# Optimization experiments

Hardware: AMD Instinct MI355X
Metric: run time of the kernel (lower is better)

## Reference

```python
import jax, jax.numpy as jnp
import numpy as np

N, H, DDE, NH = 256, 256, 64, 4

def setup_inputs() -> dict:
    key = jax.random.key(0)
    ks = jax.random.split(key, 12)
    rn = lambda k, s, sc=1.0: (jax.random.normal(k, s) * sc).astype(jnp.float32)
    return {
        "action_hidden_state": rn(ks[0], (N, H)),
        "goal_hidden_state": rn(ks[1], (N, H)),
        "goal": rn(ks[2], (N, 2)),
        "action": rn(ks[3], (N, 2)),
        "W_dist": rn(ks[4], (8, DDE), 0.3),          # distEmbedding Linear(8, dde)
        "b_dist": jnp.zeros((DDE,), jnp.float32),
        "W_gate": rn(ks[5], (DDE, H), 0.1),          # gateFC Linear(dde, H)
        "b_gate": jnp.zeros((H,), jnp.float32),
        "w": rn(ks[6], (NH, 1, H, H), 0.06),         # GAT per-head projection
        "a": rn(ks[7], (1, 1, 2 * H, 1), 0.06),      # attention vector
        "bias": jnp.zeros((H,), jnp.float32),
    }

def reference(action_hidden_state, goal_hidden_state, goal, action,
              W_dist, b_dist, W_gate, b_gate, w, a, bias):
    n = goal.shape[0]
    # --- InteractionGate.cal_gate: x1[i,j] = x[j], x2[i,j] = x[i] ---
    g1 = jnp.broadcast_to(goal[None, :, :], (n, n, 2))
    g2 = jnp.broadcast_to(goal[:, None, :], (n, n, 2))
    a1 = jnp.broadcast_to(action[None, :, :], (n, n, 2))
    a2 = jnp.broadcast_to(action[:, None, :], (n, n, 2))
    dist = jnp.concatenate([a2, g2, a1, g1], axis=-1)                 # [n,n,8]
    gate = jax.nn.sigmoid(jax.nn.relu(dist @ W_dist + b_dist) @ W_gate + b_gate)  # [n,n,H]
    # temp_action_1[i,j] = action_hidden_state[j]
    gate_action = gate * jnp.tanh(action_hidden_state[None, :, :])    # [n,n,H]
    # diagonal entries replaced by goal_hidden_state (mask_goal = eye)
    eye = jnp.eye(n, dtype=bool)[:, :, None]
    gated_h = jnp.where(eye, goal_hidden_state[None, :, :], gate_action)  # [n,n,H]

    # --- GAT assembly: h_self[i,k] = ahs[i]; h_other = cat(ahs, gated_h) ---
    h_other = jnp.concatenate([action_hidden_state[:, None, :], gated_h], axis=1)  # [n,n+1,H]

    wm = w[:, 0]          # [NH,H,H]
    a_flat = a[0, 0, :, 0]  # [2H]
    f = wm.shape[-1]
    n_head = wm.shape[0]
    # h_self rows along k are all identical -> project once per (head, node)
    hsp = jnp.einsum('nh,zhf->znf', action_hidden_state, wm)          # [NH,n,f]
    hop = jnp.einsum('nkh,zhf->znkf', h_other, wm)                    # [NH,n,n+1,f]
    # cat([h_self', h_other']) @ a  ==  h_self'@a[:f] + h_other'@a[f:]
    score = (hsp @ a_flat[:f])[:, :, None] + hop @ a_flat[f:]         # [NH,n,n+1]
    e = jnp.where(score > 0, score, 0.2 * score)                      # LeakyReLU(0.2)
    alpha = jax.nn.softmax(e, axis=-1)                                # softmax over neighbors
    # h_attn = matmul(h_other, w) == hop; weighted sum over k, mean over heads
    out = jnp.einsum('znk,znkf->nf', alpha, hop) / n_head             # [n,f]
    return jax.nn.relu(out) + bias
```

## Files before the change

kernel.cpp:

```cpp
#include <hip/hip_runtime.h>
#include <hip/hip_bf16.h>

#define NN 256
#define HH 256

typedef __attribute__((ext_vector_type(8))) short short8;
typedef __attribute__((ext_vector_type(4))) float f32x4;
typedef __attribute__((ext_vector_type(4))) unsigned short su4;

__device__ __forceinline__ ushort f2bf(float x) {
    __hip_bfloat16 h = __float2bfloat16(x);
    return *reinterpret_cast<ushort*>(&h);
}
__device__ __forceinline__ float bf2f(ushort u) {
    __hip_bfloat16 h = *reinterpret_cast<__hip_bfloat16*>(&u);
    return __bfloat162float(h);
}
template <int CTRL>
__device__ __forceinline__ float dpp_add(float x) {
    int y = __builtin_amdgcn_update_dpp(0, __float_as_int(x), CTRL, 0xF, 0xF, true);
    return x + __int_as_float(y);
}
template <int CTRL>
__device__ __forceinline__ float dpp_max(float x) {
    int y = __builtin_amdgcn_update_dpp(0, __float_as_int(x), CTRL, 0xF, 0xF, true);
    return fmaxf(x, __int_as_float(y));
}
__device__ __forceinline__ float red16(float v) {
    v = dpp_add<0xB1>(v); v = dpp_add<0x4E>(v);
    v = dpp_add<0x141>(v); v = dpp_add<0x140>(v);
    return v;
}
__device__ __forceinline__ float red16max(float v) {
    v = dpp_max<0xB1>(v); v = dpp_max<0x4E>(v);
    v = dpp_max<0x141>(v); v = dpp_max<0x140>(v);
    return v;
}

#define WS_P   0
#define WS_Q   16384
#define WS_T   32768
#define WS_WA  98304
#define WS_WB  99328
#define WS_WGT 100352
#define WS_PV  109568
#define WS_ML  1158144
#define WS_W2H 1166336
#define WS_W2L 1297408

__global__ __launch_bounds__(256) void precompute_kernel(
    const float* __restrict__ ahs, const float* __restrict__ goal,
    const float* __restrict__ action, const float* __restrict__ Wd,
    const float* __restrict__ b_dist, const float* __restrict__ Wg,
    const float* __restrict__ w, const float* __restrict__ a,
    float* __restrict__ ws)
{
    const int b = blockIdx.x;
    const int t = threadIdx.x;
    float* P  = ws + WS_P;
    float* Q  = ws + WS_Q;
    float* T  = ws + WS_T;
    float* WA = ws + WS_WA;
    float* WB = ws + WS_WB;
    ushort* WgT  = (ushort*)(ws + WS_WGT);
    ushort* W2hi = (ushort*)(ws + WS_W2H);
    ushort* W2lo = (ushort*)(ws + WS_W2L);

    __shared__ __align__(16) float tile[64][65];

    if (b < 64) {
        const int idx = (b*256 + t)*4;
        float4 v = *(const float4*)(ahs + idx);
        float4 o;
        o.x = tanhf(v.x); o.y = tanhf(v.y); o.z = tanhf(v.z); o.w = tanhf(v.w);
        *(float4*)(T + idx) = o;
    } else if (b < 128) {
        const int i = (b - 64)*4 + (t >> 6);
        const int d = t & 63;
        float a0 = action[2*i], a1 = action[2*i+1];
        float g0 = goal[2*i],   g1 = goal[2*i+1];
        P[i*64 + d] = a0*Wd[0*64+d] + a1*Wd[1*64+d]
                    + g0*Wd[2*64+d] + g1*Wd[3*64+d] + b_dist[d];
        Q[i*64 + d] = a0*Wd[4*64+d] + a1*Wd[5*64+d]
                    + g0*Wd[6*64+d] + g1*Wd[7*64+d];
    } else if (b < 144) {
        const int r    = b - 128;
        const int z    = r >> 2;
        const int rg   = r & 3;
        const int wid  = t >> 6;
        const int lane = t & 63;
        const int hbase = rg*64 + wid*16;
        const f32x4 aB = *(const f32x4*)(a + lane*4);
        const f32x4 aA = *(const f32x4*)(a + HH + lane*4);
#pragma unroll 4
        for (int rr = 0; rr < 16; ++rr) {
            const int h = hbase + rr;
            const f32x4 w4 = *(const f32x4*)(w + z*HH*HH + h*HH + lane*4);
            float dA = w4.x*aA.x + w4.y*aA.y + w4.z*aA.z + w4.w*aA.w;
            float dB = w4.x*aB.x + w4.y*aB.y + w4.z*aB.z + w4.w*aB.w;
#pragma unroll
            for (int off = 32; off; off >>= 1) {
                dA += __shfl_xor(dA, off);
                dB += __shfl_xor(dB, off);
            }
            if (lane == 0) { WA[z*HH + h] = dA; WB[z*HH + h] = dB; }
        }
    } else if (b < 208) {
        const int d = b - 144;
        WgT[t*72 + d] = f2bf(Wg[d*HH + t]);
    } else {
        const int idx = b - 208;
        const int k0  = (idx >> 2) * 64;
        const int f0  = (idx & 3) * 64;
        const int r   = t >> 6;
        const int ff  = t & 63;
#pragma unroll 4
        for (int i = 0; i < 16; ++i) {
            const int kk = i*4 + r;
            tile[kk][ff] = w[(k0 + kk)*HH + f0 + ff];
        }
        __syncthreads();
#pragma unroll 4
        for (int i = 0; i < 16; ++i) {
            const int fl = i*4 + r;
            float x = tile[ff][fl];
            ushort hi = f2bf(x);
            ushort lo = f2bf(x - bf2f(hi));
            W2hi[(size_t)(f0 + fl)*1024 + k0 + ff] = hi;
            W2lo[(size_t)(f0 + fl)*1024 + k0 + ff] = lo;
        }
    }
}

__global__ __launch_bounds__(256, 4) void gat_partial_kernel(
    const float* __restrict__ ahs, const float* __restrict__ ghs,
    const float* __restrict__ b_gate, float* __restrict__ ws)
{
    const int n    = blockIdx.x & 255;
    const int qq   = blockIdx.x >> 8;
    const int t    = threadIdx.x;
    const int wid  = t >> 6;
    const int lane = t & 63;
    const int quad = lane >> 4;
    const int l15  = lane & 15;
    const int zg   = quad;
    const int jj   = l15;
    const int n0   = wid * 64;

    const float* P  = ws + WS_P;
    const float* Q  = ws + WS_Q;
    const float* T  = ws + WS_T;
    const float* WA = ws + WS_WA;
    const float* WB = ws + WS_WB;
    const ushort* WgTg = (const ushort*)(ws + WS_WGT);
    float* PV = ws + WS_PV;
    float* ML = ws + WS_ML;

    __shared__ __align__(16) ushort wg_lds[256][72];
    __shared__ __align__(16) float part[2][4][16][4];
    __shared__ __align__(16) float alpha_w[4][16][4];
    float* vred = (float*)&wg_lds[0][0];

    {
        const short8* src = (const short8*)WgTg;
        short8* dst = (short8*)&wg_lds[0][0];
#pragma unroll
        for (int i = 0; i < 9; ++i) dst[i*256 + t] = src[i*256 + t];
    }

    int hcol[4];
#pragma unroll
    for (int nt = 0; nt < 4; ++nt) hcol[nt] = n0 + nt*16 + l15;

    float wa_reg[4][4];
    float bgv[4], gval[4];
#pragma unroll
    for (int nt = 0; nt < 4; ++nt) {
#pragma unroll
        for (int z = 0; z < 4; ++z) wa_reg[z][nt] = WA[z*HH + hcol[nt]];
        bgv[nt]  = b_gate[hcol[nt]];
        gval[nt] = ghs[n*HH + hcol[nt]];
    }

    float pnA[2][8];
#pragma unroll
    for (int kh = 0; kh < 2; ++kh) {
        *(f32x4*)&pnA[kh][0] = *(const f32x4*)(P + n*64 + kh*32 + quad*8);
        *(f32x4*)&pnA[kh][4] = *(const f32x4*)(P + n*64 + kh*32 + quad*8 + 4);
    }

    float vacc[4][4];
    {
        float av[4];
#pragma unroll
        for (int nt = 0; nt < 4; ++nt) av[nt] = ahs[n*HH + hcol[nt]];
#pragma unroll
        for (int z = 0; z < 4; ++z)
#pragma unroll
            for (int nt = 0; nt < 4; ++nt)
                vacc[z][nt] = (qq == 0 && quad == 0) ? av[nt] : 0.f;
    }

    float cz_r, m_r, l_r;
    {
        float pc = 0.f, ps = 0.f;
        const int hb = jj*16;
#pragma unroll
        for (int i4 = 0; i4 < 4; ++i4) {
            f32x4 av = *(const f32x4*)(ahs + n*HH + hb + i4*4);
            f32x4 wb = *(const f32x4*)(WB + zg*HH + hb + i4*4);
            f32x4 wa = *(const f32x4*)(WA + zg*HH + hb + i4*4);
            pc = fmaf(av.x, wb.x, pc); pc = fmaf(av.y, wb.y, pc);
            pc = fmaf(av.z, wb.z, pc); pc = fmaf(av.w, wb.w, pc);
            ps = fmaf(av.x, wa.x, ps); ps = fmaf(av.y, wa.y, ps);
            ps = fmaf(av.z, wa.z, ps); ps = fmaf(av.w, wa.w, ps);
        }
        pc = red16(pc); ps = red16(ps);
        cz_r = pc;
        if (qq == 0) {
            float sc = pc + ps;
            m_r = sc > 0.f ? sc : 0.2f * sc;
            l_r = 1.0f;
        } else {
            m_r = -__builtin_inff();
            l_r = 0.0f;
        }
    }
    __syncthreads();

    for (int cc = 0; cc < 4; ++cc) {
        const int j0  = qq*64 + cc*16;
        const int par = cc & 1;

        float tval[4][4];
#pragma unroll
        for (int r = 0; r < 4; ++r) {
            const int jg = j0 + quad*4 + r;
#pragma unroll
            for (int nt = 0; nt < 4; ++nt)
                tval[nt][r] = T[jg*HH + hcol[nt]];
        }

        short8 afrag[2];
#pragma unroll
        for (int kh = 0; kh < 2; ++kh) {
            const float* qrow = Q + (j0 + l15)*64 + kh*32 + quad*8;
            f32x4 qa = *(const f32x4*)qrow;
            f32x4 qb = *(const f32x4*)(qrow + 4);
            ushort hv[8];
            hv[0] = f2bf(fmaxf(pnA[kh][0] + qa.x, 0.f));
            hv[1] = f2bf(fmaxf(pnA[kh][1] + qa.y, 0.f));
            hv[2] = f2bf(fmaxf(pnA[kh][2] + qa.z, 0.f));
            hv[3] = f2bf(fmaxf(pnA[kh][3] + qa.w, 0.f));
            hv[4] = f2bf(fmaxf(pnA[kh][4] + qb.x, 0.f));
            hv[5] = f2bf(fmaxf(pnA[kh][5] + qb.y, 0.f));
            hv[6] = f2bf(fmaxf(pnA[kh][6] + qb.z, 0.f));
            hv[7] = f2bf(fmaxf(pnA[kh][7] + qb.w, 0.f));
            afrag[kh] = *(short8*)hv;
        }

        f32x4 acc[4];
#pragma unroll
        for (int nt = 0; nt < 4; ++nt) {
            short8 b0 = *(const short8*)&wg_lds[hcol[nt]][quad*8];
            short8 b1 = *(const short8*)&wg_lds[hcol[nt]][32 + quad*8];
            f32x4 a4 = (f32x4){0.f,0.f,0.f,0.f};
            a4 = __builtin_amdgcn_mfma_f32_16x16x32_bf16(afrag[0], b0, a4, 0, 0, 0);
            a4 = __builtin_amdgcn_mfma_f32_16x16x32_bf16(afrag[1], b1, a4, 0, 0, 0);
            acc[nt] = a4;
        }

        float vals[4][4];
#pragma unroll
        for (int r = 0; r < 4; ++r) {
            const int jg = j0 + quad*4 + r;
            const bool diag = (jg == n);
#pragma unroll
            for (int nt = 0; nt < 4; ++nt) {
                float u = acc[nt][r] + bgv[nt];
                float g = 1.0f / (1.0f + __expf(-u));
                vals[nt][r] = diag ? gval[nt] : g * tval[nt][r];
            }
        }

#pragma unroll
        for (int z = 0; z < 4; ++z) {
            float pp[4];
#pragma unroll
            for (int r = 0; r < 4; ++r) {
                float s = 0.f;
#pragma unroll
                for (int nt = 0; nt < 4; ++nt)
                    s = fmaf(vals[nt][r], wa_reg[z][nt], s);
                pp[r] = red16(s);
            }
            if (l15 == z) {
#pragma unroll
                for (int r = 0; r < 4; ++r)
                    part[par][z][quad*4 + r][wid] = pp[r];
            }
        }
        __syncthreads();

        float scl0, scl1, scl2, scl3;
        {
            f32x4 pr = *(const f32x4*)&part[par][zg][jj][0];
            float s = cz_r + ((pr.x + pr.y) + (pr.z + pr.w));
            float e = s > 0.f ? s : 0.2f * s;
            float mx = red16max(e);
            float m_new = fmaxf(m_r, mx);
            float at = __expf(e - m_new);
            float ss = red16(at);
            float scale = __expf(m_r - m_new);
            l_r = l_r * scale + ss;
            m_r = m_new;
            alpha_w[wid][jj][zg] = at;
            scl0 = __shfl(scale, 0);
            scl1 = __shfl(scale, 16);
            scl2 = __shfl(scale, 32);
            scl3 = __shfl(scale, 48);
        }
#pragma unroll
        for (int nt = 0; nt < 4; ++nt) {
            vacc[0][nt] *= scl0; vacc[1][nt] *= scl1;
            vacc[2][nt] *= scl2; vacc[3][nt] *= scl3;
        }
#pragma unroll
        for (int r = 0; r < 4; ++r) {
            f32x4 al = *(const f32x4*)&alpha_w[wid][quad*4 + r][0];
#pragma unroll
            for (int nt = 0; nt < 4; ++nt) {
                float v = vals[nt][r];
                vacc[0][nt] = fmaf(al.x, v, vacc[0][nt]);
                vacc[1][nt] = fmaf(al.y, v, vacc[1][nt]);
                vacc[2][nt] = fmaf(al.z, v, vacc[2][nt]);
                vacc[3][nt] = fmaf(al.w, v, vacc[3][nt]);
            }
        }
    }

#pragma unroll
    for (int z = 0; z < 4; ++z)
#pragma unroll
        for (int nt = 0; nt < 4; ++nt)
            vred[(quad*4 + z)*260 + hcol[nt]] = vacc[z][nt];
    __syncthreads();
#pragma unroll
    for (int z = 0; z < 4; ++z) {
        float s = (vred[(0*4+z)*260 + t] + vred[(1*4+z)*260 + t])
                + (vred[(2*4+z)*260 + t] + vred[(3*4+z)*260 + t]);
        PV[((qq*4 + z)*NN + n)*HH + t] = s;
    }
    if (wid == 0 && l15 == 0) {
        ML[((qq*4 + zg)*NN + n)*2 + 0] = m_r;
        ML[((qq*4 + zg)*NN + n)*2 + 1] = l_r;
    }
}

__global__ __launch_bounds__(256) void gat_out_kernel(
    const float* __restrict__ bias, const float* __restrict__ ws,
    float* __restrict__ out)
{
    const int n0 = (blockIdx.x >> 2) * 16;
    const int f0 = (blockIdx.x & 3) * 64;
    const int t    = threadIdx.x;
    const int wid  = t >> 6;
    const int lane = t & 63;
    const int quad = lane >> 4;
    const int l15  = lane & 15;

    const float* PV = ws + WS_PV;
    const float* ML = ws + WS_ML;
    const ushort* W2hi = (const ushort*)(ws + WS_W2H);
    const ushort* W2lo = (const ushort*)(ws + WS_W2L);

    __shared__ __align__(16) char smx[67072];
    ushort (*VNh)[1032] = (ushort(*)[1032])smx;
    ushort (*VNl)[1032] = (ushort(*)[1032])(smx + 33024);
    float  (*sq)[4][4]  = (float(*)[4][4])(smx + 66048);
    float* red = (float*)smx;

    {
        const int n_i = t >> 4, z = (t >> 2) & 3, q = t & 3;
        float m = ML[((q*4 + z)*NN + n0 + n_i)*2 + 0];
        float l = ML[((q*4 + z)*NN + n0 + n_i)*2 + 1];
        float mm = fmaxf(m, __shfl_xor(m, 1));
        mm = fmaxf(mm, __shfl_xor(mm, 2));
        float s  = __expf(m - mm);
        float ls = l * s;
        ls += __shfl_xor(ls, 1);
        ls += __shfl_xor(ls, 2);
        sq[n_i][z][q] = s / ls;
    }
    __syncthreads();

    {
        const int z  = t >> 6;
        const int kk = (t & 63) * 4;
#pragma unroll 4
        for (int n_i = 0; n_i < 16; ++n_i) {
            const int n = n0 + n_i;
            f32x4 v = (f32x4){0.f,0.f,0.f,0.f};
#pragma unroll
            for (int q = 0; q < 4; ++q) {
                float sc = sq[n_i][z][q];
                f32x4 pv = *(const f32x4*)(PV + ((size_t)(q*4 + z)*NN + n)*HH + kk);
                v.x = fmaf(sc, pv.x, v.x); v.y = fmaf(sc, pv.y, v.y);
                v.z = fmaf(sc, pv.z, v.z); v.w = fmaf(sc, pv.w, v.w);
            }
            ushort hi[4], lo[4];
#pragma unroll
            for (int c = 0; c < 4; ++c) {
                float x = ((float*)&v)[c];
                hi[c] = f2bf(x);
                lo[c] = f2bf(x - bf2f(hi[c]));
            }
            *(su4*)&VNh[n_i][z*256 + kk] = *(su4*)hi;
            *(su4*)&VNl[n_i][z*256 + kk] = *(su4*)lo;
        }
    }
    __syncthreads();

    f32x4 acc[4];
#pragma unroll
    for (int nt = 0; nt < 4; ++nt) acc[nt] = (f32x4){0.f,0.f,0.f,0.f};
    {
        const int wk0 = wid * 256;
        for (int ks = 0; ks < 8; ++ks) {
            const int k0 = wk0 + ks*32;
            short8 ah = *(const short8*)&VNh[l15][k0 + quad*8];
            short8 al = *(const short8*)&VNl[l15][k0 + quad*8];
#pragma unroll
            for (int nt = 0; nt < 4; ++nt) {
                const size_t boff = (size_t)(f0 + nt*16 + l15)*1024 + k0 + quad*8;
                short8 bh = *(const short8*)(W2hi + boff);
                short8 bl = *(const short8*)(W2lo + boff);
                acc[nt] = __builtin_amdgcn_mfma_f32_16x16x32_bf16(ah, bh, acc[nt], 0, 0, 0);
                acc[nt] = __builtin_amdgcn_mfma_f32_16x16x32_bf16(ah, bl, acc[nt], 0, 0, 0);
                acc[nt] = __builtin_amdgcn_mfma_f32_16x16x32_bf16(al, bh, acc[nt], 0, 0, 0);
            }
        }
    }
    __syncthreads();

    if (wid > 0) {
#pragma unroll
        for (int nt = 0; nt < 4; ++nt)
#pragma unroll
            for (int r = 0; r < 4; ++r)
                red[(((wid-1)*4 + nt)*16 + quad*4 + r)*16 + l15] = acc[nt][r];
    }
    __syncthreads();
    if (wid == 0) {
#pragma unroll
        for (int nt = 0; nt < 4; ++nt) {
            const int f = f0 + nt*16 + l15;
            float bv = bias[f];
#pragma unroll
            for (int r = 0; r < 4; ++r) {
                const int row = quad*4 + r;
                float s = acc[nt][r]
                        + red[((0*4 + nt)*16 + row)*16 + l15]
                        + red[((1*4 + nt)*16 + row)*16 + l15]
                        + red[((2*4 + nt)*16 + row)*16 + l15];
                out[(size_t)(n0 + row)*HH + f] = fmaxf(0.25f * s, 0.f) + bv;
            }
        }
    }
}

extern "C" void kernel_launch(void* const* d_in, const int* in_sizes, int n_in,
                              void* d_out, int out_size, void* d_ws, size_t ws_size,
                              hipStream_t stream)
{
    const float* ahs    = (const float*)d_in[0];
    const float* ghs    = (const float*)d_in[1];
    const float* goal   = (const float*)d_in[2];
    const float* action = (const float*)d_in[3];
    const float* Wd     = (const float*)d_in[4];
    const float* b_dist = (const float*)d_in[5];
    const float* Wg     = (const float*)d_in[6];
    const float* b_gate = (const float*)d_in[7];
    const float* w      = (const float*)d_in[8];
    const float* a      = (const float*)d_in[9];
    const float* bias   = (const float*)d_in[10];
    float* ws   = (float*)d_ws;
    float* outp = (float*)d_out;

    precompute_kernel<<<272, 256, 0, stream>>>(ahs, goal, action, Wd, b_dist, Wg, w, a, ws);
    gat_partial_kernel<<<1024, 256, 0, stream>>>(ahs, ghs, b_gate, ws);
    gat_out_kernel<<<64, 256, 0, stream>>>(bias, ws, outp);
}
```

Measured before the change: 128.2 us.

## Halve GAT neighbor split, keep gate weights in registers, fuse PV combine into MFMA

The neighbor dimension is now split two ways instead of four, so the partial kernel launches 512 blocks that each cover 128 neighbors, and the PV/ML workspace shrinks. Gate-weight B fragments are loaded once into registers from global memory instead of being staged through LDS. The output kernel combines the two partials straight into MFMA A fragments in registers, skipping the LDS VN staging. The precompute blocks are reordered so the long-running ones start first. In exchange, fewer blocks may lower occupancy and latency hiding, and each block holds more registers.

```diff
diff --git a/kernel.cpp b/kernel.cpp
--- a/kernel.cpp
+++ b/kernel.cpp
@@ -6,7 +6,6 @@
 
 typedef __attribute__((ext_vector_type(8))) short short8;
 typedef __attribute__((ext_vector_type(4))) float f32x4;
-typedef __attribute__((ext_vector_type(4))) unsigned short su4;
 
 __device__ __forceinline__ ushort f2bf(float x) {
     __hip_bfloat16 h = __float2bfloat16(x);
@@ -43,10 +42,10 @@
 #define WS_WA  98304
 #define WS_WB  99328
 #define WS_WGT 100352
-#define WS_PV  109568
-#define WS_ML  1158144
-#define WS_W2H 1166336
-#define WS_W2L 1297408
+#define WS_PV  108544
+#define WS_ML  632832
+#define WS_W2H 636928
+#define WS_W2L 768000
 
 __global__ __launch_bounds__(256) void precompute_kernel(
     const float* __restrict__ ahs, const float* __restrict__ goal,
@@ -57,6 +56,8 @@
 {
     const int b = blockIdx.x;
     const int t = threadIdx.x;
+    const int wid  = t >> 6;
+    const int lane = t & 63;
     float* P  = ws + WS_P;
     float* Q  = ws + WS_Q;
     float* T  = ws + WS_T;
@@ -68,27 +69,9 @@
 
     __shared__ __align__(16) float tile[64][65];
 
-    if (b < 64) {
-        const int idx = (b*256 + t)*4;
-        float4 v = *(const float4*)(ahs + idx);
-        float4 o;
-        o.x = tanhf(v.x); o.y = tanhf(v.y); o.z = tanhf(v.z); o.w = tanhf(v.w);
-        *(float4*)(T + idx) = o;
-    } else if (b < 128) {
-        const int i = (b - 64)*4 + (t >> 6);
-        const int d = t & 63;
-        float a0 = action[2*i], a1 = action[2*i+1];
-        float g0 = goal[2*i],   g1 = goal[2*i+1];
-        P[i*64 + d] = a0*Wd[0*64+d] + a1*Wd[1*64+d]
-                    + g0*Wd[2*64+d] + g1*Wd[3*64+d] + b_dist[d];
-        Q[i*64 + d] = a0*Wd[4*64+d] + a1*Wd[5*64+d]
-                    + g0*Wd[6*64+d] + g1*Wd[7*64+d];
-    } else if (b < 144) {
-        const int r    = b - 128;
-        const int z    = r >> 2;
-        const int rg   = r & 3;
-        const int wid  = t >> 6;
-        const int lane = t & 63;
+    if (b < 16) {
+        const int z  = b >> 2;
+        const int rg = b & 3;
         const int hbase = rg*64 + wid*16;
         const f32x4 aB = *(const f32x4*)(a + lane*4);
         const f32x4 aA = *(const f32x4*)(a + HH + lane*4);
@@ -105,39 +88,53 @@
             }
             if (lane == 0) { WA[z*HH + h] = dA; WB[z*HH + h] = dB; }
         }
-    } else if (b < 208) {
-        const int d = b - 144;
-        WgT[t*72 + d] = f2bf(Wg[d*HH + t]);
-    } else {
-        const int idx = b - 208;
+    } else if (b < 80) {
+        const int idx = b - 16;
         const int k0  = (idx >> 2) * 64;
         const int f0  = (idx & 3) * 64;
-        const int r   = t >> 6;
         const int ff  = t & 63;
 #pragma unroll 4
         for (int i = 0; i < 16; ++i) {
-            const int kk = i*4 + r;
+            const int kk = i*4 + wid;
             tile[kk][ff] = w[(k0 + kk)*HH + f0 + ff];
         }
         __syncthreads();
 #pragma unroll 4
         for (int i = 0; i < 16; ++i) {
-            const int fl = i*4 + r;
+            const int fl = i*4 + wid;
             float x = tile[ff][fl];
             ushort hi = f2bf(x);
             ushort lo = f2bf(x - bf2f(hi));
             W2hi[(size_t)(f0 + fl)*1024 + k0 + ff] = hi;
             W2lo[(size_t)(f0 + fl)*1024 + k0 + ff] = lo;
         }
-    }
-}
-
-__global__ __launch_bounds__(256, 4) void gat_partial_kernel(
+    } else if (b < 144) {
+        const int i = (b - 80)*4 + wid;
+        const int d = lane;
+        float a0 = action[2*i], a1 = action[2*i+1];
+        float g0 = goal[2*i],   g1 = goal[2*i+1];
+        P[i*64 + d] = a0*Wd[0*64+d] + a1*Wd[1*64+d]
+                    + g0*Wd[2*64+d] + g1*Wd[3*64+d] + b_dist[d];
+        Q[i*64 + d] = a0*Wd[4*64+d] + a1*Wd[5*64+d]
+                    + g0*Wd[6*64+d] + g1*Wd[7*64+d];
+    } else if (b < 208) {
+        const int d = b - 144;
+        WgT[t*64 + d] = f2bf(Wg[d*HH + t]);
+    } else {
+        const int idx = ((b - 208)*256 + t)*4;
+        float4 v = *(const float4*)(ahs + idx);
+        float4 o;
+        o.x = tanhf(v.x); o.y = tanhf(v.y); o.z = tanhf(v.z); o.w = tanhf(v.w);
+        *(float4*)(T + idx) = o;
+    }
+}
+
+__global__ __launch_bounds__(256, 2) void gat_partial_kernel(
     const float* __restrict__ ahs, const float* __restrict__ ghs,
     const float* __restrict__ b_gate, float* __restrict__ ws)
 {
-    const int n    = blockIdx.x & 255;
-    const int qq   = blockIdx.x >> 8;
+    const int n    = blockIdx.x >> 1;
+    const int hh   = blockIdx.x & 1;
     const int t    = threadIdx.x;
     const int wid  = t >> 6;
     const int lane = t & 63;
@@ -152,30 +149,26 @@
     const float* T  = ws + WS_T;
     const float* WA = ws + WS_WA;
     const float* WB = ws + WS_WB;
-    const ushort* WgTg = (const ushort*)(ws + WS_WGT);
+    const ushort* WgT = (const ushort*)(ws + WS_WGT);
     float* PV = ws + WS_PV;
     float* ML = ws + WS_ML;
 
-    __shared__ __align__(16) ushort wg_lds[256][72];
     __shared__ __align__(16) float part[2][4][16][4];
     __shared__ __align__(16) float alpha_w[4][16][4];
-    float* vred = (float*)&wg_lds[0][0];
-
-    {
-        const short8* src = (const short8*)WgTg;
-        short8* dst = (short8*)&wg_lds[0][0];
-#pragma unroll
-        for (int i = 0; i < 9; ++i) dst[i*256 + t] = src[i*256 + t];
-    }
+    __shared__ __align__(16) float vred[16][260];
 
     int hcol[4];
 #pragma unroll
     for (int nt = 0; nt < 4; ++nt) hcol[nt] = n0 + nt*16 + l15;
 
-    float wa_reg[4][4];
-    float bgv[4], gval[4];
+    short8 bfrag[4][2];
+    float  wa_reg[4][4];
+    float  bgv[4], gval[4];
 #pragma unroll
     for (int nt = 0; nt < 4; ++nt) {
+#pragma unroll
+        for (int kh = 0; kh < 2; ++kh)
+            bfrag[nt][kh] = *(const short8*)(WgT + hcol[nt]*64 + kh*32 + quad*8);
 #pragma unroll
         for (int z = 0; z < 4; ++z) wa_reg[z][nt] = WA[z*HH + hcol[nt]];
         bgv[nt]  = b_gate[hcol[nt]];
@@ -198,7 +191,7 @@
         for (int z = 0; z < 4; ++z)
 #pragma unroll
             for (int nt = 0; nt < 4; ++nt)
-                vacc[z][nt] = (qq == 0 && quad == 0) ? av[nt] : 0.f;
+                vacc[z][nt] = (hh == 0 && quad == 0) ? av[nt] : 0.f;
     }
 
     float cz_r, m_r, l_r;
@@ -217,7 +210,7 @@
         }
         pc = red16(pc); ps = red16(ps);
         cz_r = pc;
-        if (qq == 0) {
+        if (hh == 0) {
             float sc = pc + ps;
             m_r = sc > 0.f ? sc : 0.2f * sc;
             l_r = 1.0f;
@@ -226,10 +219,9 @@
             l_r = 0.0f;
         }
     }
-    __syncthreads();
-
-    for (int cc = 0; cc < 4; ++cc) {
-        const int j0  = qq*64 + cc*16;
+
+    for (int cc = 0; cc < 8; ++cc) {
+        const int j0  = hh*128 + cc*16;
         const int par = cc & 1;
 
         float tval[4][4];
@@ -262,11 +254,9 @@
         f32x4 acc[4];
 #pragma unroll
         for (int nt = 0; nt < 4; ++nt) {
-            short8 b0 = *(const short8*)&wg_lds[hcol[nt]][quad*8];
-            short8 b1 = *(const short8*)&wg_lds[hcol[nt]][32 + quad*8];
             f32x4 a4 = (f32x4){0.f,0.f,0.f,0.f};
-            a4 = __builtin_amdgcn_mfma_f32_16x16x32_bf16(afrag[0], b0, a4, 0, 0, 0);
-            a4 = __builtin_amdgcn_mfma_f32_16x16x32_bf16(afrag[1], b1, a4, 0, 0, 0);
+            a4 = __builtin_amdgcn_mfma_f32_16x16x32_bf16(afrag[0], bfrag[nt][0], a4, 0, 0, 0);
+            a4 = __builtin_amdgcn_mfma_f32_16x16x32_bf16(afrag[1], bfrag[nt][1], a4, 0, 0, 0);
             acc[nt] = a4;
         }
 
@@ -343,17 +333,16 @@
     for (int z = 0; z < 4; ++z)
 #pragma unroll
         for (int nt = 0; nt < 4; ++nt)
-            vred[(quad*4 + z)*260 + hcol[nt]] = vacc[z][nt];
+            vred[quad*4 + z][hcol[nt]] = vacc[z][nt];
     __syncthreads();
 #pragma unroll
     for (int z = 0; z < 4; ++z) {
-        float s = (vred[(0*4+z)*260 + t] + vred[(1*4+z)*260 + t])
-                + (vred[(2*4+z)*260 + t] + vred[(3*4+z)*260 + t]);
-        PV[((qq*4 + z)*NN + n)*HH + t] = s;
+        float s = (vred[0*4+z][t] + vred[1*4+z][t]) + (vred[2*4+z][t] + vred[3*4+z][t]);
+        PV[((size_t)(hh*4 + z)*NN + n)*HH + t] = s;
     }
     if (wid == 0 && l15 == 0) {
-        ML[((qq*4 + zg)*NN + n)*2 + 0] = m_r;
-        ML[((qq*4 + zg)*NN + n)*2 + 1] = l_r;
+        ML[((hh*4 + zg)*NN + n)*2 + 0] = m_r;
+        ML[((hh*4 + zg)*NN + n)*2 + 1] = l_r;
     }
 }
 
@@ -374,81 +363,68 @@
     const ushort* W2hi = (const ushort*)(ws + WS_W2H);
     const ushort* W2lo = (const ushort*)(ws + WS_W2L);
 
-    __shared__ __align__(16) char smx[67072];
-    ushort (*VNh)[1032] = (ushort(*)[1032])smx;
-    ushort (*VNl)[1032] = (ushort(*)[1032])(smx + 33024);
-    float  (*sq)[4][4]  = (float(*)[4][4])(smx + 66048);
-    float* red = (float*)smx;
-
-    {
-        const int n_i = t >> 4, z = (t >> 2) & 3, q = t & 3;
+    __shared__ __align__(16) float redc[12288/4];
+    __shared__ __align__(16) float sq[16][4][2];
+
+    if (t < 128) {
+        const int n_i = t >> 3, z = (t >> 1) & 3, q = t & 1;
         float m = ML[((q*4 + z)*NN + n0 + n_i)*2 + 0];
         float l = ML[((q*4 + z)*NN + n0 + n_i)*2 + 1];
         float mm = fmaxf(m, __shfl_xor(m, 1));
-        mm = fmaxf(mm, __shfl_xor(mm, 2));
         float s  = __expf(m - mm);
         float ls = l * s;
         ls += __shfl_xor(ls, 1);
-        ls += __shfl_xor(ls, 2);
         sq[n_i][z][q] = s / ls;
     }
     __syncthreads();
 
-    {
-        const int z  = t >> 6;
-        const int kk = (t & 63) * 4;
-#pragma unroll 4
-        for (int n_i = 0; n_i < 16; ++n_i) {
-            const int n = n0 + n_i;
-            f32x4 v = (f32x4){0.f,0.f,0.f,0.f};
-#pragma unroll
-            for (int q = 0; q < 4; ++q) {
-                float sc = sq[n_i][z][q];
-                f32x4 pv = *(const f32x4*)(PV + ((size_t)(q*4 + z)*NN + n)*HH + kk);
-                v.x = fmaf(sc, pv.x, v.x); v.y = fmaf(sc, pv.y, v.y);
-                v.z = fmaf(sc, pv.z, v.z); v.w = fmaf(sc, pv.w, v.w);
-            }
-            ushort hi[4], lo[4];
-#pragma unroll
-            for (int c = 0; c < 4; ++c) {
-                float x = ((float*)&v)[c];
-                hi[c] = f2bf(x);
-                lo[c] = f2bf(x - bf2f(hi[c]));
-            }
-            *(su4*)&VNh[n_i][z*256 + kk] = *(su4*)hi;
-            *(su4*)&VNl[n_i][z*256 + kk] = *(su4*)lo;
+    f32x4 acc[4];
+#pragma unroll
+    for (int nt = 0; nt < 4; ++nt) acc[nt] = (f32x4){0.f,0.f,0.f,0.f};
+
+    const float s0 = sq[l15][wid][0];
+    const float s1 = sq[l15][wid][1];
+    const float* pv0 = PV + ((size_t)(0*4 + wid)*NN + n0 + l15)*HH;
+    const float* pv1 = PV + ((size_t)(1*4 + wid)*NN + n0 + l15)*HH;
+
+    for (int ks = 0; ks < 8; ++ks) {
+        const int kp = ks*32 + quad*8;
+        f32x4 p0a = *(const f32x4*)(pv0 + kp);
+        f32x4 p0b = *(const f32x4*)(pv0 + kp + 4);
+        f32x4 p1a = *(const f32x4*)(pv1 + kp);
+        f32x4 p1b = *(const f32x4*)(pv1 + kp + 4);
+        float v[8];
+        v[0] = s0*p0a.x + s1*p1a.x; v[1] = s0*p0a.y + s1*p1a.y;
+        v[2] = s0*p0a.z + s1*p1a.z; v[3] = s0*p0a.w + s1*p1a.w;
+        v[4] = s0*p0b.x + s1*p1b.x; v[5] = s0*p0b.y + s1*p1b.y;
+        v[6] = s0*p0b.z + s1*p1b.z; v[7] = s0*p0b.w + s1*p1b.w;
+        ushort hi[8], lo[8];
+#pragma unroll
+        for (int c = 0; c < 8; ++c) {
+            hi[c] = f2bf(v[c]);
+            lo[c] = f2bf(v[c] - bf2f(hi[c]));
+        }
+        short8 ah = *(short8*)hi;
+        short8 al = *(short8*)lo;
+        const int kg = wid*256 + kp;
+#pragma unroll
+        for (int nt = 0; nt < 4; ++nt) {
+            const size_t boff = (size_t)(f0 + nt*16 + l15)*1024 + kg;
+            short8 bh = *(const short8*)(W2hi + boff);
+            short8 bl = *(const short8*)(W2lo + boff);
+            acc[nt] = __builtin_amdgcn_mfma_f32_16x16x32_bf16(ah, bh, acc[nt], 0, 0, 0);
+            acc[nt] = __builtin_amdgcn_mfma_f32_16x16x32_bf16(ah, bl, acc[nt], 0, 0, 0);
+            acc[nt] = __builtin_amdgcn_mfma_f32_16x16x32_bf16(al, bh, acc[nt], 0, 0, 0);
         }
     }
     __syncthreads();
 
-    f32x4 acc[4];
-#pragma unroll
-    for (int nt = 0; nt < 4; ++nt) acc[nt] = (f32x4){0.f,0.f,0.f,0.f};
-    {
-        const int wk0 = wid * 256;
-        for (int ks = 0; ks < 8; ++ks) {
-            const int k0 = wk0 + ks*32;
-            short8 ah = *(const short8*)&VNh[l15][k0 + quad*8];
-            short8 al = *(const short8*)&VNl[l15][k0 + quad*8];
-#pragma unroll
-            for (int nt = 0; nt < 4; ++nt) {
-                const size_t boff = (size_t)(f0 + nt*16 + l15)*1024 + k0 + quad*8;
-                short8 bh = *(const short8*)(W2hi + boff);
-                short8 bl = *(const short8*)(W2lo + boff);
-                acc[nt] = __builtin_amdgcn_mfma_f32_16x16x32_bf16(ah, bh, acc[nt], 0, 0, 0);
-                acc[nt] = __builtin_amdgcn_mfma_f32_16x16x32_bf16(ah, bl, acc[nt], 0, 0, 0);
-                acc[nt] = __builtin_amdgcn_mfma_f32_16x16x32_bf16(al, bh, acc[nt], 0, 0, 0);
-            }
-        }
-    }
-    __syncthreads();
-
     if (wid > 0) {
 #pragma unroll
         for (int nt = 0; nt < 4; ++nt)
 #pragma unroll
             for (int r = 0; r < 4; ++r)
-                red[(((wid-1)*4 + nt)*16 + quad*4 + r)*16 + l15] = acc[nt][r];
+                redc[(((wid-1)*4 + nt)*16 + quad*4 + r)*16 + l15] = acc[nt][r];
     }
     __syncthreads();
     if (wid == 0) {
@@ -460,9 +436,9 @@
             for (int r = 0; r < 4; ++r) {
                 const int row = quad*4 + r;
                 float s = acc[nt][r]
-                        + red[((0*4 + nt)*16 + row)*16 + l15]
-                        + red[((1*4 + nt)*16 + row)*16 + l15]
-                        + red[((2*4 + nt)*16 + row)*16 + l15];
+                        + redc[((0*4 + nt)*16 + row)*16 + l15]
+                        + redc[((1*4 + nt)*16 + row)*16 + l15]
+                        + redc[((2*4 + nt)*16 + row)*16 + l15];
                 out[(size_t)(n0 + row)*HH + f] = fmaxf(0.25f * s, 0.f) + bv;
             }
         }
@@ -488,6 +464,6 @@
     float* outp = (float*)d_out;
 
     precompute_kernel<<<272, 256, 0, stream>>>(ahs, goal, action, Wd, b_dist, Wg, w, a, ws);
-    gat_partial_kernel<<<1024, 256, 0, stream>>>(ahs, ghs, b_gate, ws);
+    gat_partial_kernel<<<512, 256, 0, stream>>>(ahs, ghs, b_gate, ws);
     gat_out_kernel<<<64, 256, 0, stream>>>(bias, ws, outp);
 }
```

After: 125.5 us. 1.02x faster.
